# Kernel tuning notes

Measured on AMD Instinct MI355X. Metric: run time of the kernel, lower is better.

The kernel has to match this reference:

```python
import jax, jax.numpy as jnp
import numpy as np

GROUP = 128  # per-group quantization along the input dimension


def _quantize_int4(w):
    """Asymmetric INT4 per-group quantization. w: [out, in] -> (q, scale, zero).
    q: int32 in [0,15], shape [out, in//GROUP, GROUP]; scale/zero: [out, in//GROUP]."""
    o, i = w.shape
    wg = w.reshape(o, i // GROUP, GROUP)
    mn = wg.min(axis=-1)
    mx = wg.max(axis=-1)
    scale = (mx - mn) / 15.0
    scale = jnp.where(scale == 0, jnp.float32(1.0), scale)
    zero = jnp.clip(jnp.round(-mn / scale), 0.0, 15.0)
    q = jnp.clip(jnp.round(wg / scale[..., None]) + zero[..., None], 0.0, 15.0).astype(jnp.int32)
    return q, scale.astype(jnp.float32), zero.astype(jnp.float32)


def _dequant(q, s, z):
    """(q - zero) * scale, regrouped back to [out, in]."""
    w = (q.astype(jnp.float32) - z[..., None]) * s[..., None]
    return w.reshape(q.shape[0], -1)


def setup_inputs() -> dict:
    key = jax.random.key(0)
    ks = jax.random.split(key, 5)
    B, D_IN, D_H, D_OUT = 512, 2048, 8192, 2048
    x = jax.random.normal(ks[0], (B, D_IN), dtype=jnp.float32)
    w1 = jax.random.normal(ks[1], (D_H, D_IN), dtype=jnp.float32) * 0.02
    b1 = jax.random.normal(ks[2], (D_H,), dtype=jnp.float32) * 0.01
    w2 = jax.random.normal(ks[3], (D_OUT, D_H), dtype=jnp.float32) * 0.02
    b2 = jax.random.normal(ks[4], (D_OUT,), dtype=jnp.float32) * 0.01
    q1, s1, z1 = _quantize_int4(w1)
    q2, s2, z2 = _quantize_int4(w2)
    return {"x": x, "q1": q1, "s1": s1, "z1": z1, "b1": b1,
            "q2": q2, "s2": s2, "z2": z2, "b2": b2}


def reference(x, q1, s1, z1, b1, q2, s2, z2, b2):
    # Layer 1: INT4 dequant + Linear + ReLU (fused in the native kernel)
    w1 = _dequant(q1, s1, z1)              # [D_H, D_IN]
    h = jax.nn.relu(x @ w1.T + b1)         # [B, D_H]
    # Layer 2: INT4 dequant + Linear (no activation)
    w2 = _dequant(q2, s2, z2)              # [D_OUT, D_H]
    return h @ w2.T + b2                   # [B, D_OUT]
```

## Files before the change

kernel.cpp:

```cpp
#include <hip/hip_runtime.h>
#include <stdint.h>

typedef unsigned short u16;
typedef __attribute__((ext_vector_type(8))) short bf16x8;
typedef __attribute__((ext_vector_type(8))) unsigned short u16x8;
typedef __attribute__((ext_vector_type(4))) float f32x4;
typedef __attribute__((ext_vector_type(4))) int i32x4;

__device__ __forceinline__ u16 f2bf(float f) {
  uint32_t u = __builtin_bit_cast(uint32_t, f);
  u += 0x7fffu + ((u >> 16) & 1u);
  return (u16)(u >> 16);
}

#define GLD16(g, l)                                                         \
  __builtin_amdgcn_global_load_lds(                                         \
      (const __attribute__((address_space(1))) void*)(g),                   \
      (__attribute__((address_space(3))) void*)(l), 16, 0, 0)


__global__ __launch_bounds__(256) void cvt_f32_bf16(const float* __restrict__ src,
                                                    u16* __restrict__ dst, int n8) {
  int t = blockIdx.x * 256 + threadIdx.x;
  if (t >= n8) return;
  f32x4 a = ((const f32x4*)src)[2 * t];
  f32x4 b = ((const f32x4*)src)[2 * t + 1];
  u16x8 o;
  o[0] = f2bf(a[0]); o[1] = f2bf(a[1]); o[2] = f2bf(a[2]); o[3] = f2bf(a[3]);
  o[4] = f2bf(b[0]); o[5] = f2bf(b[1]); o[6] = f2bf(b[2]); o[7] = f2bf(b[3]);
  ((u16x8*)dst)[t] = o;
}

__global__ __launch_bounds__(256) void dequant_w(const int* __restrict__ q,
                                                 const float* __restrict__ s,
                                                 const float* __restrict__ z,
                                                 u16* __restrict__ w, int n8) {
  int t = blockIdx.x * 256 + threadIdx.x;
  if (t >= n8) return;
  int g = t >> 4;
  float sc = s[g];
  float zp = z[g];
  i32x4 a = ((const i32x4*)q)[2 * t];
  i32x4 b = ((const i32x4*)q)[2 * t + 1];
  u16x8 o;
  o[0] = f2bf(((float)a[0] - zp) * sc);
  o[1] = f2bf(((float)a[1] - zp) * sc);
  o[2] = f2bf(((float)a[2] - zp) * sc);
  o[3] = f2bf(((float)a[3] - zp) * sc);
  o[4] = f2bf(((float)b[0] - zp) * sc);
  o[5] = f2bf(((float)b[1] - zp) * sc);
  o[6] = f2bf(((float)b[2] - zp) * sc);
  o[7] = f2bf(((float)b[3] - zp) * sc);
  ((u16x8*)w)[t] = o;
}

__global__ __launch_bounds__(256) void bias_init(float* __restrict__ out,
                                                 const float* __restrict__ b,
                                                 int N, int n4) {
  int t = blockIdx.x * 256 + threadIdx.x;
  if (t >= n4) return;
  int idx = t * 4;
  int n = idx & (N - 1);
  *(f32x4*)(out + idx) = *(const f32x4*)(b + n);
}

template <bool RELU, bool OUT_BF16, bool ATOMIC>
__global__ __launch_bounds__(256) void gemm_bt(const u16* __restrict__ A,
                                               const u16* __restrict__ Bm,
                                               const float* __restrict__ bias,
                                               void* __restrict__ Cout,
                                               int M, int N, int K, int kChunk) {
  __shared__ u16 As[3][128 * 32];
  __shared__ u16 Bs[3][128 * 32];
  const int tid = threadIdx.x;
  const int wave = tid >> 6;
  const int lane = tid & 63;
  const int m0 = blockIdx.y << 7;
  const int n0 = blockIdx.x << 7;
  const int kStart = blockIdx.z * kChunk;
  const int srow = lane >> 2;
  const int scol = (((lane & 3) ^ ((lane >> 3) & 3)) << 3);
  const int wm = (wave >> 1) << 6;
  const int wn = (wave & 1) << 6;
  const int quad = lane >> 4;
  const int l15 = lane & 15;
  const int cs = ((quad ^ ((l15 >> 1) & 3)) << 3);

  const u16* Ab = A + (size_t)(m0 + 32 * wave + srow) * K + kStart + scol;
  const u16* Bb = Bm + (size_t)(n0 + 32 * wave + srow) * K + kStart + scol;
  const int ldsW = (32 * wave) * 32;
  const size_t rowskip = (size_t)16 * K;
  const int nT = kChunk >> 5;

  f32x4 acc[4][4];
#pragma unroll
  for (int i = 0; i < 4; i++)
#pragma unroll
    for (int j = 0; j < 4; j++) acc[i][j] = (f32x4){0.f, 0.f, 0.f, 0.f};

#define STAGE(bi_, t_)                                    \
  do {                                                    \
    const int ko_ = (t_) << 5;                            \
    GLD16(Ab + ko_, &As[bi_][ldsW]);                      \
    GLD16(Ab + ko_ + rowskip, &As[bi_][ldsW + 512]);      \
    GLD16(Bb + ko_, &Bs[bi_][ldsW]);                      \
    GLD16(Bb + ko_ + rowskip, &Bs[bi_][ldsW + 512]);      \
  } while (0)

  bf16x8 af[4], bf[4];
#define LOADFRAGS(bi_)                                                        \
  do {                                                                        \
    _Pragma("unroll") for (int i = 0; i < 4; i++)                             \
        af[i] = *(const bf16x8*)&As[bi_][(wm + i * 16 + l15) * 32 + cs];      \
    _Pragma("unroll") for (int j = 0; j < 4; j++)                             \
        bf[j] = *(const bf16x8*)&Bs[bi_][(wn + j * 16 + l15) * 32 + cs];      \
  } while (0)

#define DOMFMA()                                                              \
  do {                                                                        \
    _Pragma("unroll") for (int i = 0; i < 4; i++)                             \
        _Pragma("unroll") for (int j = 0; j < 4; j++)                         \
            acc[i][j] = __builtin_amdgcn_mfma_f32_16x16x32_bf16(              \
                af[i], bf[j], acc[i][j], 0, 0, 0);                            \
  } while (0)

  STAGE(0, 0);
  STAGE(1, 1);
  STAGE(2, 2);

  int bi = 0;
  for (int t = 0; t < nT - 2; ++t) {
    asm volatile("s_waitcnt vmcnt(8)" ::: "memory");
    __builtin_amdgcn_s_barrier();
    LOADFRAGS(bi);
    asm volatile("s_waitcnt lgkmcnt(0)" ::: "memory");
    __builtin_amdgcn_s_barrier();
    if (t + 3 < nT) STAGE(bi, t + 3);
    DOMFMA();
    bi = (bi == 2) ? 0 : bi + 1;
  }
  asm volatile("s_waitcnt vmcnt(4)" ::: "memory");
  __builtin_amdgcn_s_barrier();
  LOADFRAGS(bi);
  DOMFMA();
  bi = (bi == 2) ? 0 : bi + 1;
  asm volatile("s_waitcnt vmcnt(0)" ::: "memory");
  __builtin_amdgcn_s_barrier();
  LOADFRAGS(bi);
  DOMFMA();

#undef STAGE
#undef LOADFRAGS
#undef DOMFMA

#pragma unroll
  for (int i = 0; i < 4; i++) {
#pragma unroll
    for (int j = 0; j < 4; j++) {
      const int col = n0 + wn + j * 16 + l15;
      float bv = 0.f;
      if (!ATOMIC) bv = bias[col];
#pragma unroll
      for (int r = 0; r < 4; r++) {
        const int row = m0 + wm + i * 16 + quad * 4 + r;
        float v = acc[i][j][r];
        if (ATOMIC) {
          atomicAdd((float*)Cout + (size_t)row * N + col, v);
        } else {
          v += bv;
          if (RELU) v = v > 0.f ? v : 0.f;
          if (OUT_BF16)
            ((u16*)Cout)[(size_t)row * N + col] = f2bf(v);
          else
            ((float*)Cout)[(size_t)row * N + col] = v;
        }
      }
    }
  }
}


extern "C" void kernel_launch(void* const* d_in, const int* in_sizes, int n_in,
                              void* d_out, int out_size, void* d_ws, size_t ws_size,
                              hipStream_t stream) {
  const float* x  = (const float*)d_in[0];
  const int*   q1 = (const int*)d_in[1];
  const float* s1 = (const float*)d_in[2];
  const float* z1 = (const float*)d_in[3];
  const float* b1 = (const float*)d_in[4];
  const int*   q2 = (const int*)d_in[5];
  const float* s2 = (const float*)d_in[6];
  const float* z2 = (const float*)d_in[7];
  const float* b2 = (const float*)d_in[8];
  float* out = (float*)d_out;

  const int B = 512, D_IN = 2048, D_H = 8192, D_OUT = 2048;

  char* ws = (char*)d_ws;
  u16* xb  = (u16*)(ws);
  u16* w1b = (u16*)(ws + (size_t)2 * 1024 * 1024);
  u16* hb  = (u16*)(ws + (size_t)34 * 1024 * 1024);
  u16* w2b = (u16*)(ws + (size_t)42 * 1024 * 1024);

  cvt_f32_bf16<<<(B * D_IN / 8 + 255) / 256, 256, 0, stream>>>(x, xb, B * D_IN / 8);
  dequant_w<<<(D_H * D_IN / 8 + 255) / 256, 256, 0, stream>>>(q1, s1, z1, w1b, D_H * D_IN / 8);
  dequant_w<<<(D_OUT * D_H / 8 + 255) / 256, 256, 0, stream>>>(q2, s2, z2, w2b, D_OUT * D_H / 8);
  dim3 g1(D_H / 128, B / 128, 1);
  gemm_bt<true, true, false><<<g1, 256, 0, stream>>>(xb, w1b, b1, hb, B, D_H, D_IN, D_IN);
  bias_init<<<(B * D_OUT / 4 + 255) / 256, 256, 0, stream>>>(out, b2, D_OUT, B * D_OUT / 4);
  dim3 g2(D_OUT / 128, B / 128, 8);
  gemm_bt<false, false, true><<<g2, 256, 0, stream>>>(hb, w2b, nullptr, out, B, D_OUT, D_H, D_H / 8);
}
```

Before: 252.9 us.

## Use BK=64 double-buffered GEMM with split LDS waits and merge dequant launches

The GEMM k-tile grows from 32 to 64 and the pipeline goes from a triple buffer to a double buffer. Fragment loads are split into two k-halves, so the MFMAs for the first half start while the second half's LDS reads are still in flight, with the next stage's global loads issued in between. The swizzle changes to an 8-chunk XOR pattern to match the wider rows. The two weight-dequant launches are merged into one grid with z=2, saving a launch. The risk is shallower prefetch, since only one tile is outstanding, and tighter wait-count correctness.

```diff
diff --git a/kernel.cpp b/kernel.cpp
--- a/kernel.cpp
+++ b/kernel.cpp
@@ -31,12 +31,20 @@
   ((u16x8*)dst)[t] = o;
 }
 
-__global__ __launch_bounds__(256) void dequant_w(const int* __restrict__ q,
-                                                 const float* __restrict__ s,
-                                                 const float* __restrict__ z,
-                                                 u16* __restrict__ w, int n8) {
+__global__ __launch_bounds__(256) void dequant_w2x(const int* __restrict__ qa,
+                                                   const float* __restrict__ sa,
+                                                   const float* __restrict__ za,
+                                                   u16* __restrict__ wa,
+                                                   const int* __restrict__ qb,
+                                                   const float* __restrict__ sb,
+                                                   const float* __restrict__ zb,
+                                                   u16* __restrict__ wb, int n8) {
   int t = blockIdx.x * 256 + threadIdx.x;
   if (t >= n8) return;
+  const int* q = blockIdx.z ? qb : qa;
+  const float* s = blockIdx.z ? sb : sa;
+  const float* z = blockIdx.z ? zb : za;
+  u16* w = blockIdx.z ? wb : wa;
   int g = t >> 4;
   float sc = s[g];
   float zp = z[g];
@@ -70,27 +78,29 @@
                                                const float* __restrict__ bias,
                                                void* __restrict__ Cout,
                                                int M, int N, int K, int kChunk) {
-  __shared__ u16 As[3][128 * 32];
-  __shared__ u16 Bs[3][128 * 32];
+  __shared__ u16 As[2][128 * 64];
+  __shared__ u16 Bs[2][128 * 64];
   const int tid = threadIdx.x;
   const int wave = tid >> 6;
   const int lane = tid & 63;
   const int m0 = blockIdx.y << 7;
   const int n0 = blockIdx.x << 7;
   const int kStart = blockIdx.z * kChunk;
-  const int srow = lane >> 2;
-  const int scol = (((lane & 3) ^ ((lane >> 3) & 3)) << 3);
+  const int srow = lane >> 3;
+  const int schunk = (((lane & 7) ^ (srow & 7)) << 3);
   const int wm = (wave >> 1) << 6;
   const int wn = (wave & 1) << 6;
   const int quad = lane >> 4;
   const int l15 = lane & 15;
-  const int cs = ((quad ^ ((l15 >> 1) & 3)) << 3);
-
-  const u16* Ab = A + (size_t)(m0 + 32 * wave + srow) * K + kStart + scol;
-  const u16* Bb = Bm + (size_t)(n0 + 32 * wave + srow) * K + kStart + scol;
-  const int ldsW = (32 * wave) * 32;
-  const size_t rowskip = (size_t)16 * K;
-  const int nT = kChunk >> 5;
+  const int x7 = lane & 7;
+  const int c0 = ((quad ^ x7) << 3);
+  const int c1 = (((4 | quad) ^ x7) << 3);
+
+  const u16* Ab = A + (size_t)(m0 + 32 * wave + srow) * K + kStart + schunk;
+  const u16* Bb = Bm + (size_t)(n0 + 32 * wave + srow) * K + kStart + schunk;
+  const int ldsW = (32 * wave) * 64;
+  const size_t rs8 = (size_t)8 * K;
+  const int nT = kChunk >> 6;
 
   f32x4 acc[4][4];
 #pragma unroll
@@ -98,60 +108,90 @@
 #pragma unroll
     for (int j = 0; j < 4; j++) acc[i][j] = (f32x4){0.f, 0.f, 0.f, 0.f};
 
-#define STAGE(bi_, t_)                                    \
-  do {                                                    \
-    const int ko_ = (t_) << 5;                            \
-    GLD16(Ab + ko_, &As[bi_][ldsW]);                      \
-    GLD16(Ab + ko_ + rowskip, &As[bi_][ldsW + 512]);      \
-    GLD16(Bb + ko_, &Bs[bi_][ldsW]);                      \
-    GLD16(Bb + ko_ + rowskip, &Bs[bi_][ldsW + 512]);      \
-  } while (0)
-
-  bf16x8 af[4], bf[4];
-#define LOADFRAGS(bi_)                                                        \
-  do {                                                                        \
-    _Pragma("unroll") for (int i = 0; i < 4; i++)                             \
-        af[i] = *(const bf16x8*)&As[bi_][(wm + i * 16 + l15) * 32 + cs];      \
-    _Pragma("unroll") for (int j = 0; j < 4; j++)                             \
-        bf[j] = *(const bf16x8*)&Bs[bi_][(wn + j * 16 + l15) * 32 + cs];      \
-  } while (0)
-
-#define DOMFMA()                                                              \
-  do {                                                                        \
-    _Pragma("unroll") for (int i = 0; i < 4; i++)                             \
-        _Pragma("unroll") for (int j = 0; j < 4; j++)                         \
-            acc[i][j] = __builtin_amdgcn_mfma_f32_16x16x32_bf16(              \
-                af[i], bf[j], acc[i][j], 0, 0, 0);                            \
+#define STAGE(bi_, t_)                                          \
+  do {                                                          \
+    const int ko_ = (t_) << 6;                                  \
+    GLD16(Ab + ko_,           &As[bi_][ldsW]);                  \
+    GLD16(Ab + ko_ + rs8,     &As[bi_][ldsW + 512]);            \
+    GLD16(Ab + ko_ + 2 * rs8, &As[bi_][ldsW + 1024]);           \
+    GLD16(Ab + ko_ + 3 * rs8, &As[bi_][ldsW + 1536]);           \
+    GLD16(Bb + ko_,           &Bs[bi_][ldsW]);                  \
+    GLD16(Bb + ko_ + rs8,     &Bs[bi_][ldsW + 512]);            \
+    GLD16(Bb + ko_ + 2 * rs8, &Bs[bi_][ldsW + 1024]);           \
+    GLD16(Bb + ko_ + 3 * rs8, &Bs[bi_][ldsW + 1536]);           \
+  } while (0)
+
+  bf16x8 af0[4], bf0[4], af1[4], bf1[4];
+#define LOADFRAGS(bi_)                                                          \
+  do {                                                                          \
+    _Pragma("unroll") for (int i = 0; i < 4; i++)                               \
+        af0[i] = *(const bf16x8*)&As[bi_][(wm + i * 16 + l15) * 64 + c0];       \
+    _Pragma("unroll") for (int j = 0; j < 4; j++)                               \
+        bf0[j] = *(const bf16x8*)&Bs[bi_][(wn + j * 16 + l15) * 64 + c0];       \
+    _Pragma("unroll") for (int i = 0; i < 4; i++)                               \
+        af1[i] = *(const bf16x8*)&As[bi_][(wm + i * 16 + l15) * 64 + c1];       \
+    _Pragma("unroll") for (int j = 0; j < 4; j++)                               \
+        bf1[j] = *(const bf16x8*)&Bs[bi_][(wn + j * 16 + l15) * 64 + c1];       \
+  } while (0)
+
+#define MFMA_S0()                                                               \
+  do {                                                                          \
+    _Pragma("unroll") for (int i = 0; i < 4; i++)                               \
+        _Pragma("unroll") for (int j = 0; j < 4; j++)                           \
+            acc[i][j] = __builtin_amdgcn_mfma_f32_16x16x32_bf16(                \
+                af0[i], bf0[j], acc[i][j], 0, 0, 0);                            \
+  } while (0)
+
+#define MFMA_S1()                                                               \
+  do {                                                                          \
+    _Pragma("unroll") for (int i = 0; i < 4; i++)                               \
+        _Pragma("unroll") for (int j = 0; j < 4; j++)                           \
+            acc[i][j] = __builtin_amdgcn_mfma_f32_16x16x32_bf16(                \
+                af1[i], bf1[j], acc[i][j], 0, 0, 0);                            \
   } while (0)
 
   STAGE(0, 0);
   STAGE(1, 1);
-  STAGE(2, 2);
 
   int bi = 0;
   for (int t = 0; t < nT - 2; ++t) {
     asm volatile("s_waitcnt vmcnt(8)" ::: "memory");
     __builtin_amdgcn_s_barrier();
     LOADFRAGS(bi);
+    asm volatile("s_waitcnt lgkmcnt(8)" ::: "memory");
+    __builtin_amdgcn_sched_barrier(0);
+    MFMA_S0();
     asm volatile("s_waitcnt lgkmcnt(0)" ::: "memory");
+    __builtin_amdgcn_sched_barrier(0);
     __builtin_amdgcn_s_barrier();
-    if (t + 3 < nT) STAGE(bi, t + 3);
-    DOMFMA();
-    bi = (bi == 2) ? 0 : bi + 1;
+    STAGE(bi, t + 2);
+    MFMA_S1();
+    bi ^= 1;
   }
-  asm volatile("s_waitcnt vmcnt(4)" ::: "memory");
+  asm volatile("s_waitcnt vmcnt(8)" ::: "memory");
   __builtin_amdgcn_s_barrier();
   LOADFRAGS(bi);
-  DOMFMA();
-  bi = (bi == 2) ? 0 : bi + 1;
+  asm volatile("s_waitcnt lgkmcnt(8)" ::: "memory");
+  __builtin_amdgcn_sched_barrier(0);
+  MFMA_S0();
+  asm volatile("s_waitcnt lgkmcnt(0)" ::: "memory");
+  __builtin_amdgcn_sched_barrier(0);
+  MFMA_S1();
+  bi ^= 1;
   asm volatile("s_waitcnt vmcnt(0)" ::: "memory");
   __builtin_amdgcn_s_barrier();
   LOADFRAGS(bi);
-  DOMFMA();
+  asm volatile("s_waitcnt lgkmcnt(8)" ::: "memory");
+  __builtin_amdgcn_sched_barrier(0);
+  MFMA_S0();
+  asm volatile("s_waitcnt lgkmcnt(0)" ::: "memory");
+  __builtin_amdgcn_sched_barrier(0);
+  MFMA_S1();
 
 #undef STAGE
 #undef LOADFRAGS
-#undef DOMFMA
+#undef MFMA_S0
+#undef MFMA_S1
 
 #pragma unroll
   for (int i = 0; i < 4; i++) {
@@ -203,8 +243,11 @@
   u16* w2b = (u16*)(ws + (size_t)42 * 1024 * 1024);
 
   cvt_f32_bf16<<<(B * D_IN / 8 + 255) / 256, 256, 0, stream>>>(x, xb, B * D_IN / 8);
-  dequant_w<<<(D_H * D_IN / 8 + 255) / 256, 256, 0, stream>>>(q1, s1, z1, w1b, D_H * D_IN / 8);
-  dequant_w<<<(D_OUT * D_H / 8 + 255) / 256, 256, 0, stream>>>(q2, s2, z2, w2b, D_OUT * D_H / 8);
+  {
+    const int n8 = D_H * D_IN / 8;
+    dim3 gd((n8 + 255) / 256, 1, 2);
+    dequant_w2x<<<gd, 256, 0, stream>>>(q1, s1, z1, w1b, q2, s2, z2, w2b, n8);
+  }
   dim3 g1(D_H / 128, B / 128, 1);
   gemm_bt<true, true, false><<<g1, 256, 0, stream>>>(xb, w1b, b1, hb, B, D_H, D_IN, D_IN);
   bias_init<<<(B * D_OUT / 4 + 255) / 256, 256, 0, stream>>>(out, b2, D_OUT, B * D_OUT / 4);
```

Result: faster. 244.2 us (-3.4%).

## Use 256x256 split-K GEMM tiles for both layers with atomic accumulation

Applied to the files above, without the earlier changes.

Replaces the 128x128 GEMM with a 512-thread 256x256 tile kernel using double-buffered LDS, and applies split-K with atomic adds to both layers. Layer 1 now accumulates into an fp32 buffer seeded with bias, and a separate ReLU+bf16 conversion kernel follows. The larger tiles raise operand reuse per LDS load, and split-K keeps enough blocks in flight. In exchange it adds atomic traffic, an extra fp32 intermediate round-trip and extra launches, and it reuses the w1 buffer for w2.

```diff
diff --git a/kernel.cpp b/kernel.cpp
--- a/kernel.cpp
+++ b/kernel.cpp
@@ -64,24 +64,39 @@
   *(f32x4*)(out + idx) = *(const f32x4*)(b + n);
 }
 
-template <bool RELU, bool OUT_BF16, bool ATOMIC>
-__global__ __launch_bounds__(256) void gemm_bt(const u16* __restrict__ A,
-                                               const u16* __restrict__ Bm,
-                                               const float* __restrict__ bias,
-                                               void* __restrict__ Cout,
-                                               int M, int N, int K, int kChunk) {
-  __shared__ u16 As[3][128 * 32];
-  __shared__ u16 Bs[3][128 * 32];
+__global__ __launch_bounds__(256) void relu_cvt(const float* __restrict__ h32,
+                                                u16* __restrict__ hb, int n8) {
+  int t = blockIdx.x * 256 + threadIdx.x;
+  if (t >= n8) return;
+  f32x4 a = ((const f32x4*)h32)[2 * t];
+  f32x4 b = ((const f32x4*)h32)[2 * t + 1];
+  u16x8 o;
+#pragma unroll
+  for (int e = 0; e < 4; e++) {
+    float va = a[e] > 0.f ? a[e] : 0.f;
+    float vb = b[e] > 0.f ? b[e] : 0.f;
+    o[e] = f2bf(va);
+    o[e + 4] = f2bf(vb);
+  }
+  ((u16x8*)hb)[t] = o;
+}
+
+__global__ __launch_bounds__(512, 2) void gemm256_at(const u16* __restrict__ A,
+                                                     const u16* __restrict__ Bm,
+                                                     float* __restrict__ Cout,
+                                                     int N, int K, int kChunk) {
+  __shared__ u16 As[2][256 * 32];
+  __shared__ u16 Bs[2][256 * 32];
   const int tid = threadIdx.x;
   const int wave = tid >> 6;
   const int lane = tid & 63;
-  const int m0 = blockIdx.y << 7;
-  const int n0 = blockIdx.x << 7;
+  const int m0 = blockIdx.y << 8;
+  const int n0 = blockIdx.x << 8;
   const int kStart = blockIdx.z * kChunk;
   const int srow = lane >> 2;
   const int scol = (((lane & 3) ^ ((lane >> 3) & 3)) << 3);
-  const int wm = (wave >> 1) << 6;
-  const int wn = (wave & 1) << 6;
+  const int wm = (wave >> 2) << 7;
+  const int wn = (wave & 3) << 6;
   const int quad = lane >> 4;
   const int l15 = lane & 15;
   const int cs = ((quad ^ ((l15 >> 1) & 3)) << 3);
@@ -92,9 +107,9 @@
   const size_t rowskip = (size_t)16 * K;
   const int nT = kChunk >> 5;
 
-  f32x4 acc[4][4];
-#pragma unroll
-  for (int i = 0; i < 4; i++)
+  f32x4 acc[8][4];
+#pragma unroll
+  for (int i = 0; i < 8; i++)
 #pragma unroll
     for (int j = 0; j < 4; j++) acc[i][j] = (f32x4){0.f, 0.f, 0.f, 0.f};
 
@@ -107,10 +122,10 @@
     GLD16(Bb + ko_ + rowskip, &Bs[bi_][ldsW + 512]);      \
   } while (0)
 
-  bf16x8 af[4], bf[4];
+  bf16x8 af[8], bf[4];
 #define LOADFRAGS(bi_)                                                        \
   do {                                                                        \
-    _Pragma("unroll") for (int i = 0; i < 4; i++)                             \
+    _Pragma("unroll") for (int i = 0; i < 8; i++)                             \
         af[i] = *(const bf16x8*)&As[bi_][(wm + i * 16 + l15) * 32 + cs];      \
     _Pragma("unroll") for (int j = 0; j < 4; j++)                             \
         bf[j] = *(const bf16x8*)&Bs[bi_][(wn + j * 16 + l15) * 32 + cs];      \
@@ -118,7 +133,7 @@
 
 #define DOMFMA()                                                              \
   do {                                                                        \
-    _Pragma("unroll") for (int i = 0; i < 4; i++)                             \
+    _Pragma("unroll") for (int i = 0; i < 8; i++)                             \
         _Pragma("unroll") for (int j = 0; j < 4; j++)                         \
             acc[i][j] = __builtin_amdgcn_mfma_f32_16x16x32_bf16(              \
                 af[i], bf[j], acc[i][j], 0, 0, 0);                            \
@@ -126,27 +141,28 @@
 
   STAGE(0, 0);
   STAGE(1, 1);
-  STAGE(2, 2);
-
-  int bi = 0;
+
   for (int t = 0; t < nT - 2; ++t) {
-    asm volatile("s_waitcnt vmcnt(8)" ::: "memory");
+    asm volatile("s_waitcnt vmcnt(4)" ::: "memory");
     __builtin_amdgcn_s_barrier();
-    LOADFRAGS(bi);
+    LOADFRAGS(t & 1);
     asm volatile("s_waitcnt lgkmcnt(0)" ::: "memory");
+    __builtin_amdgcn_sched_barrier(0);
     __builtin_amdgcn_s_barrier();
-    if (t + 3 < nT) STAGE(bi, t + 3);
+    STAGE(t & 1, t + 2);
     DOMFMA();
-    bi = (bi == 2) ? 0 : bi + 1;
   }
   asm volatile("s_waitcnt vmcnt(4)" ::: "memory");
   __builtin_amdgcn_s_barrier();
-  LOADFRAGS(bi);
+  LOADFRAGS(nT & 1);
+  asm volatile("s_waitcnt lgkmcnt(0)" ::: "memory");
+  __builtin_amdgcn_sched_barrier(0);
   DOMFMA();
-  bi = (bi == 2) ? 0 : bi + 1;
   asm volatile("s_waitcnt vmcnt(0)" ::: "memory");
   __builtin_amdgcn_s_barrier();
-  LOADFRAGS(bi);
+  LOADFRAGS((nT - 1) & 1);
+  asm volatile("s_waitcnt lgkmcnt(0)" ::: "memory");
+  __builtin_amdgcn_sched_barrier(0);
   DOMFMA();
 
 #undef STAGE
@@ -154,26 +170,14 @@
 #undef DOMFMA
 
 #pragma unroll
-  for (int i = 0; i < 4; i++) {
+  for (int i = 0; i < 8; i++) {
 #pragma unroll
     for (int j = 0; j < 4; j++) {
       const int col = n0 + wn + j * 16 + l15;
-      float bv = 0.f;
-      if (!ATOMIC) bv = bias[col];
 #pragma unroll
       for (int r = 0; r < 4; r++) {
         const int row = m0 + wm + i * 16 + quad * 4 + r;
-        float v = acc[i][j][r];
-        if (ATOMIC) {
-          atomicAdd((float*)Cout + (size_t)row * N + col, v);
-        } else {
-          v += bv;
-          if (RELU) v = v > 0.f ? v : 0.f;
-          if (OUT_BF16)
-            ((u16*)Cout)[(size_t)row * N + col] = f2bf(v);
-          else
-            ((float*)Cout)[(size_t)row * N + col] = v;
-        }
+        atomicAdd(Cout + (size_t)row * N + col, acc[i][j][r]);
       }
     }
   }
@@ -197,17 +201,24 @@
   const int B = 512, D_IN = 2048, D_H = 8192, D_OUT = 2048;
 
   char* ws = (char*)d_ws;
-  u16* xb  = (u16*)(ws);
-  u16* w1b = (u16*)(ws + (size_t)2 * 1024 * 1024);
-  u16* hb  = (u16*)(ws + (size_t)34 * 1024 * 1024);
-  u16* w2b = (u16*)(ws + (size_t)42 * 1024 * 1024);
+  u16*   xb  = (u16*)(ws);
+  u16*   w1b = (u16*)(ws + (size_t)2 * 1024 * 1024);
+  u16*   w2b = w1b;
+  float* h32 = (float*)(ws + (size_t)34 * 1024 * 1024);
+  u16*   hb  = (u16*)(ws + (size_t)50 * 1024 * 1024);
 
   cvt_f32_bf16<<<(B * D_IN / 8 + 255) / 256, 256, 0, stream>>>(x, xb, B * D_IN / 8);
   dequant_w<<<(D_H * D_IN / 8 + 255) / 256, 256, 0, stream>>>(q1, s1, z1, w1b, D_H * D_IN / 8);
+  bias_init<<<(B * D_H / 4 + 255) / 256, 256, 0, stream>>>(h32, b1, D_H, B * D_H / 4);
+  {
+    dim3 g1(D_H / 256, B / 256, 4);
+    gemm256_at<<<g1, 512, 0, stream>>>(xb, w1b, h32, D_H, D_IN, D_IN / 4);
+  }
+  relu_cvt<<<(B * D_H / 8 + 255) / 256, 256, 0, stream>>>(h32, hb, B * D_H / 8);
   dequant_w<<<(D_OUT * D_H / 8 + 255) / 256, 256, 0, stream>>>(q2, s2, z2, w2b, D_OUT * D_H / 8);
-  dim3 g1(D_H / 128, B / 128, 1);
-  gemm_bt<true, true, false><<<g1, 256, 0, stream>>>(xb, w1b, b1, hb, B, D_H, D_IN, D_IN);
   bias_init<<<(B * D_OUT / 4 + 255) / 256, 256, 0, stream>>>(out, b2, D_OUT, B * D_OUT / 4);
-  dim3 g2(D_OUT / 128, B / 128, 8);
-  gemm_bt<false, false, true><<<g2, 256, 0, stream>>>(hb, w2b, nullptr, out, B, D_OUT, D_H, D_H / 8);
-}
+  {
+    dim3 g2(D_OUT / 256, B / 256, 16);
+    gemm256_at<<<g2, 512, 0, stream>>>(hb, w2b, out, D_OUT, D_H, D_H / 16);
+  }
+}
```

New measurement: 322.5 us. +27.5%, slower.
